# Kernel optimization log

Measured on AMD Instinct MI355X. Metric: run time of the kernel, lower is better.

The kernel has to match this reference:

```python
import jax, jax.numpy as jnp
import numpy as np

N_NODES = 50000
N_EDGES = 800000
IN_DIM = 512
HID_DIM = 128


def setup_inputs() -> dict:
    key = jax.random.key(0)
    k1, k2, k3 = jax.random.split(key, 3)
    x = jax.random.normal(k1, (N_NODES, IN_DIM), dtype=jnp.float32)
    edge_index = jax.random.randint(k2, (2, N_EDGES), 0, N_NODES, dtype=jnp.int32)
    # GCNConv weight (glorot-ish scale) and bias
    W = jax.random.normal(k3, (IN_DIM, HID_DIM), dtype=jnp.float32) * (1.0 / np.sqrt(IN_DIM))
    b = jnp.zeros((HID_DIM,), dtype=jnp.float32)
    # PReLU per-channel slope, torch default init 0.25
    prelu_w = jnp.full((HID_DIM,), 0.25, dtype=jnp.float32)
    return {"x": x, "edge_index": edge_index, "W": W, "b": b, "prelu_w": prelu_w}


def reference(x, edge_index, W, b, prelu_w):
    N = x.shape[0]
    # 1) linear transform first (GCNConv transforms then aggregates)
    h = x @ W  # [N, H]
    # 2) add self-loops
    loop = jnp.arange(N, dtype=edge_index.dtype)
    src = jnp.concatenate([edge_index[0], loop])  # [E+N]
    dst = jnp.concatenate([edge_index[1], loop])  # [E+N]
    # 3) symmetric degree normalization deg^-1/2 (self-loops guarantee deg>=1)
    deg = jax.ops.segment_sum(jnp.ones_like(dst, dtype=h.dtype), dst, num_segments=N)
    dinv = jax.lax.rsqrt(deg)
    norm = dinv[src] * dinv[dst]  # [E+N]
    # 4) gather-scale-scatter aggregation
    msg = h[src] * norm[:, None]  # [E+N, H]
    out = jax.ops.segment_sum(msg, dst, num_segments=N) + b  # [N, H]
    # 5) per-channel PReLU
    return jnp.where(out > 0, out, prelu_w * out)
```

## Files before the change

### kernel.cpp

```cpp
#include <hip/hip_runtime.h>

#define IN_DIM 512
#define HID 128
#define BK 64

#define RANGE 98
#define NB_ 511
#define NBLK 200
#define SEGCAP 2048

typedef float f4 __attribute__((ext_vector_type(4)));
typedef short bf8 __attribute__((ext_vector_type(8)));

__device__ inline unsigned short f2bf(float f) {
    unsigned u = __float_as_uint(f);
    unsigned r = (u + 0x7FFFu + ((u >> 16) & 1u)) >> 16;
    return (unsigned short)r;
}
__device__ inline float bf2f(unsigned short u) {
    return __uint_as_float(((unsigned)u) << 16);
}
__device__ inline int xcd_perm(int blk) {
    return (blk & 7) * (NBLK / 8) + (blk >> 3);
}

__global__ __launch_bounds__(256) void k_count(const int* __restrict__ dst,
                                               int* __restrict__ cmat, int E) {
    __shared__ int bins[NB_];
    const int blk = blockIdx.x, t = threadIdx.x;
    const int chunk = (((E + NBLK - 1) / NBLK) + 3) & ~3;
    const int start = blk * chunk;
    const int end = min(E, start + chunk);
    for (int i = t; i < NB_; i += 256) bins[i] = 0;
    __syncthreads();
    if (start < E) {
        int nvec = (end - start) >> 2;
        for (int i = t; i < nvec; i += 256) {
            int4 d4 = *(const int4*)(dst + start + i * 4);
            atomicAdd(&bins[d4.x / RANGE], 1);
            atomicAdd(&bins[d4.y / RANGE], 1);
            atomicAdd(&bins[d4.z / RANGE], 1);
            atomicAdd(&bins[d4.w / RANGE], 1);
        }
        for (int i = start + nvec * 4 + t; i < end; i += 256)
            atomicAdd(&bins[dst[i] / RANGE], 1);
    }
    __syncthreads();
    const int p = xcd_perm(blk);
    for (int j = t; j < NB_; j += 256) cmat[j * NBLK + p] = bins[j];
}

__global__ __launch_bounds__(256) void k_cscan(int* __restrict__ cmat,
                                               int* __restrict__ tot) {
    __shared__ int s[256];
    const int j = blockIdx.x, t = threadIdx.x;
    int v = (t < NBLK) ? cmat[j * NBLK + t] : 0;
    s[t] = v;
    __syncthreads();
    for (int off = 1; off < 256; off <<= 1) {
        int y = (t >= off) ? s[t - off] : 0;
        __syncthreads();
        s[t] += y;
        __syncthreads();
    }
    if (t < NBLK) cmat[j * NBLK + t] = s[t] - v;
    if (t == 255) tot[j] = s[255];
}

__global__ __launch_bounds__(512) void k_tscan(const int* __restrict__ tot,
                                               int* __restrict__ bbase,
                                               int* __restrict__ rowStart,
                                               int N, int E) {
    __shared__ int s[512];
    int t = threadIdx.x;
    int v = (t < NB_) ? tot[t] : 0;
    s[t] = v;
    __syncthreads();
    for (int off = 1; off < 512; off <<= 1) {
        int y = (t >= off) ? s[t - off] : 0;
        __syncthreads();
        s[t] += y;
        __syncthreads();
    }
    if (t < NB_) bbase[t] = s[t] - v;
    if (t == 0) rowStart[N] = E;
}

__global__ __launch_bounds__(256) void k_scatter(const int* __restrict__ src,
                                                 const int* __restrict__ dst,
                                                 const int* __restrict__ cmat,
                                                 const int* __restrict__ bbase,
                                                 unsigned* __restrict__ ebuf, int E) {
    __shared__ int cur[NB_];
    const int blk = blockIdx.x, t = threadIdx.x;
    const int p = xcd_perm(blk);
    for (int j = t; j < NB_; j += 256) cur[j] = bbase[j] + cmat[j * NBLK + p];
    __syncthreads();
    const int chunk = (((E + NBLK - 1) / NBLK) + 3) & ~3;
    const int start = blk * chunk;
    const int end = min(E, start + chunk);
    if (start >= E) return;
    int nvec = (end - start) >> 2;
    for (int i = t; i < nvec; i += 256) {
        int4 s4 = *(const int4*)(src + start + i * 4);
        int4 d4 = *(const int4*)(dst + start + i * 4);
        int ss[4] = {s4.x, s4.y, s4.z, s4.w};
        int dd[4] = {d4.x, d4.y, d4.z, d4.w};
#pragma unroll
        for (int k = 0; k < 4; k++) {
            int b = dd[k] / RANGE;
            int ld = dd[k] - b * RANGE;
            int pos = atomicAdd(&cur[b], 1);
            ebuf[pos] = ((unsigned)ld << 25) | (unsigned)ss[k];
        }
    }
    for (int i = start + nvec * 4 + t; i < end; i += 256) {
        int d = dst[i];
        int b = d / RANGE;
        int ld = d - b * RANGE;
        int pos = atomicAdd(&cur[b], 1);
        ebuf[pos] = ((unsigned)ld << 25) | (unsigned)src[i];
    }
}

__global__ __launch_bounds__(256) void k_binfill(const unsigned* __restrict__ ebuf,
                                                 const int* __restrict__ tot,
                                                 const int* __restrict__ bbase,
                                                 int* __restrict__ rowStart,
                                                 float* __restrict__ dinv,
                                                 int* __restrict__ esrc, int N) {
    __shared__ int bins[RANGE];
    __shared__ int cur[RANGE];
    __shared__ int ss[128];
    __shared__ int seg[SEGCAP];
    const int b = blockIdx.x;
    const int t = threadIdx.x;
    const int base = bbase[b];
    const int cnt = min(tot[b], SEGCAP);
    const int n0 = b * RANGE;
    const unsigned* ep = ebuf + base;

    for (int i = t; i < RANGE; i += 256) bins[i] = 0;
    __syncthreads();
    for (int i = t; i < cnt; i += 256) atomicAdd(&bins[ep[i] >> 25], 1);
    __syncthreads();
    int v = (t < RANGE) ? bins[t] : 0;
    if (t < 128) ss[t] = v;
    __syncthreads();
    for (int off = 1; off < 128; off <<= 1) {
        int y = (t >= off && t < 128) ? ss[t - off] : 0;
        __syncthreads();
        if (t < 128) ss[t] += y;
        __syncthreads();
    }
    if (t < RANGE) {
        int ex = ss[t] - v;
        cur[t] = ex;
        int g = n0 + t;
        if (g < N) {
            rowStart[g] = base + ex;
            dinv[g] = rsqrtf((float)(v + 1));
        }
    }
    __syncthreads();
    for (int i = t; i < cnt; i += 256) {
        unsigned w = ep[i];
        int r = atomicAdd(&cur[w >> 25], 1);
        if (r < SEGCAP) seg[r] = (int)(w & 0x1FFFFFFu);
    }
    __syncthreads();
    for (int i = t; i < cnt; i += 256) esrc[base + i] = seg[i];
}

__global__ __launch_bounds__(256) void k_convW(const float* __restrict__ W,
                                               unsigned short* __restrict__ Wt) {
    int id = blockIdx.x * 256 + threadIdx.x;
    int n = id & (HID - 1);
    int k = id >> 7;
    Wt[(size_t)n * IN_DIM + k] = f2bf(W[(size_t)k * HID + n]);
}

__global__ __launch_bounds__(256, 2) void k_gemm(const float* __restrict__ x,
                                                 const unsigned short* __restrict__ Wt,
                                                 const float* __restrict__ dinv,
                                                 unsigned short* __restrict__ h, int M) {
    __shared__ unsigned short As[128][BK + 8];
    __shared__ unsigned short Bs[128][BK + 8];
    const int t = threadIdx.x;
    const int wave = t >> 6, lane = t & 63;
    const int row0 = blockIdx.x * 128;
    const int quad = lane >> 4, l16 = lane & 15;

    f4 acc[2][8];
#pragma unroll
    for (int i = 0; i < 2; i++)
#pragma unroll
        for (int j = 0; j < 8; j++) acc[i][j] = (f4){0.f, 0.f, 0.f, 0.f};

    const int srow = t >> 1;
    const int shalf = t & 1;
    const bool rowok = (row0 + srow) < M;
    const float* xrow = x + (size_t)(row0 + srow) * IN_DIM + shalf * 32;
    const unsigned short* wrow = Wt + (size_t)srow * IN_DIM + shalf * 32;

    for (int k0 = 0; k0 < IN_DIM; k0 += BK) {
        float4 v[8];
#pragma unroll
        for (int i = 0; i < 8; i++)
            v[i] = rowok ? *(const float4*)(xrow + k0 + i * 4)
                         : make_float4(0.f, 0.f, 0.f, 0.f);
        unsigned short tmp[32];
#pragma unroll
        for (int i = 0; i < 8; i++) {
            tmp[i * 4 + 0] = f2bf(v[i].x);
            tmp[i * 4 + 1] = f2bf(v[i].y);
            tmp[i * 4 + 2] = f2bf(v[i].z);
            tmp[i * 4 + 3] = f2bf(v[i].w);
        }
#pragma unroll
        for (int i = 0; i < 4; i++)
            *(float4*)&As[srow][shalf * 32 + i * 8] = *(float4*)&tmp[i * 8];
#pragma unroll
        for (int i = 0; i < 4; i++)
            *(float4*)&Bs[srow][shalf * 32 + i * 8] =
                *(const float4*)(wrow + k0 + i * 8);
        __syncthreads();

#pragma unroll
        for (int ks = 0; ks < BK; ks += 32) {
            bf8 af[2];
#pragma unroll
            for (int rt = 0; rt < 2; rt++)
                af[rt] = *(const bf8*)&As[wave * 32 + rt * 16 + l16][ks + quad * 8];
#pragma unroll
            for (int nt = 0; nt < 8; nt++) {
                bf8 bfv = *(const bf8*)&Bs[nt * 16 + l16][ks + quad * 8];
#pragma unroll
                for (int rt = 0; rt < 2; rt++)
                    acc[rt][nt] = __builtin_amdgcn_mfma_f32_16x16x32_bf16(
                        af[rt], bfv, acc[rt][nt], 0, 0, 0);
            }
        }
        __syncthreads();
    }

#pragma unroll
    for (int rt = 0; rt < 2; rt++) {
#pragma unroll
        for (int reg = 0; reg < 4; reg++) {
            int row = row0 + wave * 32 + rt * 16 + quad * 4 + reg;
            if (row < M) {
                float dv = dinv[row];
#pragma unroll
                for (int nt = 0; nt < 8; nt++) {
                    int col = nt * 16 + l16;
                    h[(size_t)row * HID + col] = f2bf(acc[rt][nt][reg] * dv);
                }
            }
        }
    }
}

__global__ __launch_bounds__(256) void k_pull(const unsigned short* __restrict__ h,
                                              const int* __restrict__ esrc,
                                              const int* __restrict__ rowStart,
                                              const float* __restrict__ dinv,
                                              const float* __restrict__ bias,
                                              const float* __restrict__ pw,
                                              float* __restrict__ out, int N) {
    int gid = blockIdx.x * 256 + threadIdx.x;
    int node = gid >> 4;
    int l = threadIdx.x & 15;
    if (node >= N) return;
    int e0 = rowStart[node], e1 = rowStart[node + 1];
    float di = dinv[node];
    const int ci = l * 8;
    bf8 hv = *(const bf8*)&h[(size_t)node * HID + ci];
    float a[8];
#pragma unroll
    for (int c = 0; c < 8; c++) a[c] = bf2f((unsigned short)hv[c]);
    int j = e0;
    for (; j + 4 <= e1; j += 4) {
        int s0 = esrc[j], s1 = esrc[j + 1], s2 = esrc[j + 2], s3 = esrc[j + 3];
        bf8 r0 = *(const bf8*)&h[(size_t)s0 * HID + ci];
        bf8 r1 = *(const bf8*)&h[(size_t)s1 * HID + ci];
        bf8 r2 = *(const bf8*)&h[(size_t)s2 * HID + ci];
        bf8 r3 = *(const bf8*)&h[(size_t)s3 * HID + ci];
#pragma unroll
        for (int c = 0; c < 8; c++)
            a[c] += bf2f((unsigned short)r0[c]) + bf2f((unsigned short)r1[c]) +
                    bf2f((unsigned short)r2[c]) + bf2f((unsigned short)r3[c]);
    }
    for (; j < e1; j++) {
        int s = esrc[j];
        bf8 r = *(const bf8*)&h[(size_t)s * HID + ci];
#pragma unroll
        for (int c = 0; c < 8; c++) a[c] += bf2f((unsigned short)r[c]);
    }
    float4 b0 = *(const float4*)&bias[ci];
    float4 b1 = *(const float4*)&bias[ci + 4];
    float4 p0 = *(const float4*)&pw[ci];
    float4 p1 = *(const float4*)&pw[ci + 4];
    float ob[8] = {b0.x, b0.y, b0.z, b0.w, b1.x, b1.y, b1.z, b1.w};
    float op[8] = {p0.x, p0.y, p0.z, p0.w, p1.x, p1.y, p1.z, p1.w};
    float o[8];
#pragma unroll
    for (int c = 0; c < 8; c++) {
        float v = a[c] * di + ob[c];
        o[c] = v > 0.f ? v : op[c] * v;
    }
    *(float4*)&out[(size_t)node * HID + ci]     = make_float4(o[0], o[1], o[2], o[3]);
    *(float4*)&out[(size_t)node * HID + ci + 4] = make_float4(o[4], o[5], o[6], o[7]);
}

extern "C" void kernel_launch(void* const* d_in, const int* in_sizes, int n_in,
                              void* d_out, int out_size, void* d_ws, size_t ws_size,
                              hipStream_t stream) {
    const float* x  = (const float*)d_in[0];
    const int*   ei = (const int*)d_in[1];
    const float* W  = (const float*)d_in[2];
    const float* b  = (const float*)d_in[3];
    const float* pw = (const float*)d_in[4];

    const int N = in_sizes[0] / IN_DIM;
    const int E = in_sizes[1] / 2;
    const int* src = ei;
    const int* dst = ei + E;

    char* ws = (char*)d_ws;
    size_t off = 0;
    auto carve = [&](size_t bytes) -> void* {
        void* p = ws + off;
        off = (off + bytes + 255) & ~(size_t)255;
        return p;
    };
    unsigned short* h = (unsigned short*)carve((size_t)N * HID * sizeof(unsigned short));
    int*   rowStart = (int*)carve((size_t)(N + 1) * sizeof(int));
    float* dinv     = (float*)carve((size_t)N * sizeof(float));
    int*   esrc     = (int*)carve((size_t)E * sizeof(int));
    unsigned short* Wt = (unsigned short*)carve((size_t)IN_DIM * HID * sizeof(unsigned short));
    int*   cmat     = (int*)carve((size_t)NB_ * NBLK * sizeof(int));
    int*   tot      = (int*)carve((size_t)NB_ * sizeof(int));
    int*   bbase    = (int*)carve((size_t)NB_ * sizeof(int));
    unsigned* ebuf  = (unsigned*)carve((size_t)E * sizeof(unsigned));

    k_convW<<<(IN_DIM * HID) / 256, 256, 0, stream>>>(W, Wt);
    k_count<<<NBLK, 256, 0, stream>>>(dst, cmat, E);
    k_cscan<<<NB_, 256, 0, stream>>>(cmat, tot);
    k_tscan<<<1, 512, 0, stream>>>(tot, bbase, rowStart, N, E);
    k_scatter<<<NBLK, 256, 0, stream>>>(src, dst, cmat, bbase, ebuf, E);
    k_binfill<<<NB_, 256, 0, stream>>>(ebuf, tot, bbase, rowStart, dinv, esrc, N);
    k_gemm<<<(N + 127) / 128, 256, 0, stream>>>(x, Wt, dinv, h, N);
    k_pull<<<(int)(((size_t)N * 16 + 255) / 256), 256, 0, stream>>>(
        h, esrc, rowStart, dinv, b, pw, (float*)d_out, N);
}
```

Before: 235.9 us.

## Fuse CSR-build kernels into one cooperative kernel with grid syncs

Merges the weight conversion, bucket count, column scan, total scan, scatter and per-bucket fill kernels into a single cooperative launch of 511 blocks, using grid-wide syncs between phases. This removes five kernel launch gaps and lets every phase use the same block count, so the count matrix becomes 511x511. In exchange it relies on all 511 blocks being co-resident. Each phase now runs at one block per bucket with more per-block shared memory, and the scans are serialized through grid barriers.

```diff
diff --git a/kernel.cpp b/kernel.cpp
--- a/kernel.cpp
+++ b/kernel.cpp
@@ -1,4 +1,7 @@
 #include <hip/hip_runtime.h>
+#include <hip/hip_cooperative_groups.h>
+
+namespace cg = cooperative_groups;
 
 #define IN_DIM 512
 #define HID 128
@@ -6,7 +9,6 @@
 
 #define RANGE 98
 #define NB_ 511
-#define NBLK 200
 #define SEGCAP 2048
 
 typedef float f4 __attribute__((ext_vector_type(4)));
@@ -20,17 +22,40 @@
 __device__ inline float bf2f(unsigned short u) {
     return __uint_as_float(((unsigned)u) << 16);
 }
-__device__ inline int xcd_perm(int blk) {
-    return (blk & 7) * (NBLK / 8) + (blk >> 3);
-}
-
-__global__ __launch_bounds__(256) void k_count(const int* __restrict__ dst,
-                                               int* __restrict__ cmat, int E) {
+
+__device__ inline void scan512(int* s, int t) {
+    for (int off = 1; off < 512; off <<= 1) {
+        int a = (t >= off) ? s[t - off] : 0;
+        int b = (t + 256 >= off) ? s[t + 256 - off] : 0;
+        __syncthreads();
+        s[t] += a;
+        s[t + 256] += b;
+        __syncthreads();
+    }
+}
+
+__global__ __launch_bounds__(256) void k_coop(
+    const int* __restrict__ src, const int* __restrict__ dst,
+    const float* __restrict__ W, unsigned short* __restrict__ Wt,
+    int* __restrict__ cmat, int* __restrict__ tot, int* __restrict__ bbase,
+    int* __restrict__ rowStart, float* __restrict__ dinv,
+    int* __restrict__ esrc, unsigned* __restrict__ ebuf, int E, int N) {
+    cg::grid_group grid = cg::this_grid();
     __shared__ int bins[NB_];
+    __shared__ int s512[512];
+    __shared__ int cur[NB_];
+    __shared__ int seg[SEGCAP];
+
     const int blk = blockIdx.x, t = threadIdx.x;
-    const int chunk = (((E + NBLK - 1) / NBLK) + 3) & ~3;
+    const int chunk = (((E + NB_ - 1) / NB_) + 3) & ~3;
     const int start = blk * chunk;
     const int end = min(E, start + chunk);
+
+    for (int i = blk * 256 + t; i < IN_DIM * HID; i += NB_ * 256) {
+        int n = i & (HID - 1);
+        int k = i >> 7;
+        Wt[(size_t)n * IN_DIM + k] = f2bf(W[(size_t)k * HID + n]);
+    }
     for (int i = t; i < NB_; i += 256) bins[i] = 0;
     __syncthreads();
     if (start < E) {
@@ -46,138 +71,101 @@
             atomicAdd(&bins[dst[i] / RANGE], 1);
     }
     __syncthreads();
-    const int p = xcd_perm(blk);
-    for (int j = t; j < NB_; j += 256) cmat[j * NBLK + p] = bins[j];
-}
-
-__global__ __launch_bounds__(256) void k_cscan(int* __restrict__ cmat,
-                                               int* __restrict__ tot) {
-    __shared__ int s[256];
-    const int j = blockIdx.x, t = threadIdx.x;
-    int v = (t < NBLK) ? cmat[j * NBLK + t] : 0;
-    s[t] = v;
+    for (int j = t; j < NB_; j += 256) cmat[j * NB_ + blk] = bins[j];
+    grid.sync();
+
+    {
+        const int j = blk;
+        int v0 = (t < NB_) ? cmat[j * NB_ + t] : 0;
+        int v1 = (t + 256 < NB_) ? cmat[j * NB_ + t + 256] : 0;
+        s512[t] = v0;
+        s512[t + 256] = v1;
+        __syncthreads();
+        scan512(s512, t);
+        if (t < NB_) cmat[j * NB_ + t] = s512[t] - v0;
+        if (t + 256 < NB_) cmat[j * NB_ + t + 256] = s512[t + 256] - v1;
+        if (t == 0) tot[j] = s512[511];
+    }
+    grid.sync();
+
+    if (blk == 0) {
+        int v0 = (t < NB_) ? tot[t] : 0;
+        int v1 = (t + 256 < NB_) ? tot[t + 256] : 0;
+        s512[t] = v0;
+        s512[t + 256] = v1;
+        __syncthreads();
+        scan512(s512, t);
+        if (t < NB_) bbase[t] = s512[t] - v0;
+        if (t + 256 < NB_) bbase[t + 256] = s512[t + 256] - v1;
+        if (t == 0) rowStart[N] = E;
+    }
+    grid.sync();
+
+    for (int j = t; j < NB_; j += 256) cur[j] = bbase[j] + cmat[j * NB_ + blk];
     __syncthreads();
-    for (int off = 1; off < 256; off <<= 1) {
-        int y = (t >= off) ? s[t - off] : 0;
-        __syncthreads();
-        s[t] += y;
-        __syncthreads();
-    }
-    if (t < NBLK) cmat[j * NBLK + t] = s[t] - v;
-    if (t == 255) tot[j] = s[255];
-}
-
-__global__ __launch_bounds__(512) void k_tscan(const int* __restrict__ tot,
-                                               int* __restrict__ bbase,
-                                               int* __restrict__ rowStart,
-                                               int N, int E) {
-    __shared__ int s[512];
-    int t = threadIdx.x;
-    int v = (t < NB_) ? tot[t] : 0;
-    s[t] = v;
-    __syncthreads();
-    for (int off = 1; off < 512; off <<= 1) {
-        int y = (t >= off) ? s[t - off] : 0;
-        __syncthreads();
-        s[t] += y;
-        __syncthreads();
-    }
-    if (t < NB_) bbase[t] = s[t] - v;
-    if (t == 0) rowStart[N] = E;
-}
-
-__global__ __launch_bounds__(256) void k_scatter(const int* __restrict__ src,
-                                                 const int* __restrict__ dst,
-                                                 const int* __restrict__ cmat,
-                                                 const int* __restrict__ bbase,
-                                                 unsigned* __restrict__ ebuf, int E) {
-    __shared__ int cur[NB_];
-    const int blk = blockIdx.x, t = threadIdx.x;
-    const int p = xcd_perm(blk);
-    for (int j = t; j < NB_; j += 256) cur[j] = bbase[j] + cmat[j * NBLK + p];
-    __syncthreads();
-    const int chunk = (((E + NBLK - 1) / NBLK) + 3) & ~3;
-    const int start = blk * chunk;
-    const int end = min(E, start + chunk);
-    if (start >= E) return;
-    int nvec = (end - start) >> 2;
-    for (int i = t; i < nvec; i += 256) {
-        int4 s4 = *(const int4*)(src + start + i * 4);
-        int4 d4 = *(const int4*)(dst + start + i * 4);
-        int ss[4] = {s4.x, s4.y, s4.z, s4.w};
-        int dd[4] = {d4.x, d4.y, d4.z, d4.w};
-#pragma unroll
-        for (int k = 0; k < 4; k++) {
-            int b = dd[k] / RANGE;
-            int ld = dd[k] - b * RANGE;
+    if (start < E) {
+        int nvec = (end - start) >> 2;
+        for (int i = t; i < nvec; i += 256) {
+            int4 s4 = *(const int4*)(src + start + i * 4);
+            int4 d4 = *(const int4*)(dst + start + i * 4);
+            int ss4[4] = {s4.x, s4.y, s4.z, s4.w};
+            int dd4[4] = {d4.x, d4.y, d4.z, d4.w};
+#pragma unroll
+            for (int k = 0; k < 4; k++) {
+                int b = dd4[k] / RANGE;
+                int ld = dd4[k] - b * RANGE;
+                int pos = atomicAdd(&cur[b], 1);
+                ebuf[pos] = ((unsigned)ld << 25) | (unsigned)ss4[k];
+            }
+        }
+        for (int i = start + nvec * 4 + t; i < end; i += 256) {
+            int d = dst[i];
+            int b = d / RANGE;
+            int ld = d - b * RANGE;
             int pos = atomicAdd(&cur[b], 1);
-            ebuf[pos] = ((unsigned)ld << 25) | (unsigned)ss[k];
-        }
-    }
-    for (int i = start + nvec * 4 + t; i < end; i += 256) {
-        int d = dst[i];
-        int b = d / RANGE;
-        int ld = d - b * RANGE;
-        int pos = atomicAdd(&cur[b], 1);
-        ebuf[pos] = ((unsigned)ld << 25) | (unsigned)src[i];
-    }
-}
-
-__global__ __launch_bounds__(256) void k_binfill(const unsigned* __restrict__ ebuf,
-                                                 const int* __restrict__ tot,
-                                                 const int* __restrict__ bbase,
-                                                 int* __restrict__ rowStart,
-                                                 float* __restrict__ dinv,
-                                                 int* __restrict__ esrc, int N) {
-    __shared__ int bins[RANGE];
-    __shared__ int cur[RANGE];
-    __shared__ int ss[128];
-    __shared__ int seg[SEGCAP];
-    const int b = blockIdx.x;
-    const int t = threadIdx.x;
-    const int base = bbase[b];
-    const int cnt = min(tot[b], SEGCAP);
-    const int n0 = b * RANGE;
-    const unsigned* ep = ebuf + base;
-
-    for (int i = t; i < RANGE; i += 256) bins[i] = 0;
-    __syncthreads();
-    for (int i = t; i < cnt; i += 256) atomicAdd(&bins[ep[i] >> 25], 1);
-    __syncthreads();
-    int v = (t < RANGE) ? bins[t] : 0;
-    if (t < 128) ss[t] = v;
-    __syncthreads();
-    for (int off = 1; off < 128; off <<= 1) {
-        int y = (t >= off && t < 128) ? ss[t - off] : 0;
-        __syncthreads();
-        if (t < 128) ss[t] += y;
-        __syncthreads();
-    }
-    if (t < RANGE) {
-        int ex = ss[t] - v;
-        cur[t] = ex;
-        int g = n0 + t;
-        if (g < N) {
-            rowStart[g] = base + ex;
-            dinv[g] = rsqrtf((float)(v + 1));
-        }
-    }
-    __syncthreads();
-    for (int i = t; i < cnt; i += 256) {
-        unsigned w = ep[i];
-        int r = atomicAdd(&cur[w >> 25], 1);
-        if (r < SEGCAP) seg[r] = (int)(w & 0x1FFFFFFu);
-    }
-    __syncthreads();
-    for (int i = t; i < cnt; i += 256) esrc[base + i] = seg[i];
-}
-
-__global__ __launch_bounds__(256) void k_convW(const float* __restrict__ W,
-                                               unsigned short* __restrict__ Wt) {
-    int id = blockIdx.x * 256 + threadIdx.x;
-    int n = id & (HID - 1);
-    int k = id >> 7;
-    Wt[(size_t)n * IN_DIM + k] = f2bf(W[(size_t)k * HID + n]);
+            ebuf[pos] = ((unsigned)ld << 25) | (unsigned)src[i];
+        }
+    }
+    grid.sync();
+
+    {
+        const int b = blk;
+        const int base = bbase[b];
+        const int cnt = min(tot[b], SEGCAP);
+        const int n0 = b * RANGE;
+        const unsigned* ep = ebuf + base;
+
+        for (int i = t; i < RANGE; i += 256) bins[i] = 0;
+        __syncthreads();
+        for (int i = t; i < cnt; i += 256) atomicAdd(&bins[ep[i] >> 25], 1);
+        __syncthreads();
+        int v = (t < RANGE) ? bins[t] : 0;
+        if (t < 128) s512[t] = v;
+        __syncthreads();
+        for (int off = 1; off < 128; off <<= 1) {
+            int y = (t >= off && t < 128) ? s512[t - off] : 0;
+            __syncthreads();
+            if (t < 128) s512[t] += y;
+            __syncthreads();
+        }
+        if (t < RANGE) {
+            int ex = s512[t] - v;
+            cur[t] = ex;
+            int g = n0 + t;
+            if (g < N) {
+                rowStart[g] = base + ex;
+                dinv[g] = rsqrtf((float)(v + 1));
+            }
+        }
+        __syncthreads();
+        for (int i = t; i < cnt; i += 256) {
+            unsigned w = ep[i];
+            int r = atomicAdd(&cur[w >> 25], 1);
+            if (r < SEGCAP) seg[r] = (int)(w & 0x1FFFFFFu);
+        }
+        __syncthreads();
+        for (int i = t; i < cnt; i += 256) esrc[base + i] = seg[i];
+    }
 }
 
 __global__ __launch_bounds__(256, 2) void k_gemm(const float* __restrict__ x,
@@ -339,17 +327,18 @@
     float* dinv     = (float*)carve((size_t)N * sizeof(float));
     int*   esrc     = (int*)carve((size_t)E * sizeof(int));
     unsigned short* Wt = (unsigned short*)carve((size_t)IN_DIM * HID * sizeof(unsigned short));
-    int*   cmat     = (int*)carve((size_t)NB_ * NBLK * sizeof(int));
+    int*   cmat     = (int*)carve((size_t)NB_ * NB_ * sizeof(int));
     int*   tot      = (int*)carve((size_t)NB_ * sizeof(int));
     int*   bbase    = (int*)carve((size_t)NB_ * sizeof(int));
     unsigned* ebuf  = (unsigned*)carve((size_t)E * sizeof(unsigned));
 
-    k_convW<<<(IN_DIM * HID) / 256, 256, 0, stream>>>(W, Wt);
-    k_count<<<NBLK, 256, 0, stream>>>(dst, cmat, E);
-    k_cscan<<<NB_, 256, 0, stream>>>(cmat, tot);
-    k_tscan<<<1, 512, 0, stream>>>(tot, bbase, rowStart, N, E);
-    k_scatter<<<NBLK, 256, 0, stream>>>(src, dst, cmat, bbase, ebuf, E);
-    k_binfill<<<NB_, 256, 0, stream>>>(ebuf, tot, bbase, rowStart, dinv, esrc, N);
+    int E_ = E, N_ = N;
+    void* args[] = {(void*)&src, (void*)&dst, (void*)&W, (void*)&Wt,
+                    (void*)&cmat, (void*)&tot, (void*)&bbase, (void*)&rowStart,
+                    (void*)&dinv, (void*)&esrc, (void*)&ebuf,
+                    (void*)&E_, (void*)&N_};
+    hipLaunchCooperativeKernel((const void*)k_coop, dim3(NB_), dim3(256),
+                               args, 0, stream);
     k_gemm<<<(N + 127) / 128, 256, 0, stream>>>(x, Wt, dinv, h, N);
     k_pull<<<(int)(((size_t)N * 16 + 255) / 256), 256, 0, stream>>>(
         h, esrc, rowStart, dinv, b, pw, (float*)d_out, N);
```

New measurement: 478.2 us. +102.7%, slower.
